# Performance work log

Measured on AMD Instinct MI355X. Metric: run time of the kernel, lower is better.

## Reference

```python
import jax, jax.numpy as jnp
import numpy as np

N, E, G = 50000, 500000, 64
DIN, ED, H1, H2, HD, OUT = 128, 32, 256, 128, 64, 8


def setup_inputs() -> dict:
    key = jax.random.key(0)
    ks = jax.random.split(key, 20)
    g = lambda i, shape: (jax.random.normal(ks[i], shape, jnp.float32) * 0.05)
    return dict(
        node_attr=jax.random.normal(ks[0], (N, DIN), jnp.float32),
        edge_attr=jax.random.normal(ks[1], (E, ED), jnp.float32),
        edge_src=jax.random.randint(ks[2], (E,), 0, N, jnp.int32),
        edge_dst=jax.random.randint(ks[3], (E,), 0, N, jnp.int32),
        batch=jnp.sort(jax.random.randint(ks[4], (N,), 0, G, jnp.int32)),
        Wl1=g(5, (DIN, H1)), bl1=jnp.zeros((H1,), jnp.float32),
        Wr1=g(6, (DIN, H1)), br1=jnp.zeros((H1,), jnp.float32),
        We1=g(7, (ED, H1)), att1=g(8, (H1,)), b1=jnp.zeros((H1,), jnp.float32),
        Wl2=g(9, (H1, H2)), bl2=jnp.zeros((H2,), jnp.float32),
        Wr2=g(10, (H1, H2)), br2=jnp.zeros((H2,), jnp.float32),
        We2=g(11, (ED, H2)), att2=g(12, (H2,)), b2=jnp.zeros((H2,), jnp.float32),
        Wd1=g(13, (H2, HD)), bd1=jnp.zeros((HD,), jnp.float32),
        bn_gamma=jnp.ones((HD,), jnp.float32), bn_beta=jnp.zeros((HD,), jnp.float32),
        bn_mean=jnp.zeros((HD,), jnp.float32), bn_var=jnp.ones((HD,), jnp.float32),
        Wd2=g(14, (HD, OUT)), bd2=jnp.zeros((OUT,), jnp.float32),
    )


def gatv2(x, src, dst, eattr, Wl, bl, Wr, br, We, att, bias, n):
    # PyG GATv2Conv, heads=1: add self-loops (fill_value='mean' for edge_attr)
    ones = jnp.ones((eattr.shape[0],), x.dtype)
    deg = jax.ops.segment_sum(ones, dst, n)
    loop_attr = jax.ops.segment_sum(eattr, dst, n) / jnp.maximum(deg, 1.0)[:, None]
    loop = jnp.arange(n, dtype=src.dtype)
    src_ = jnp.concatenate([src, loop])
    dst_ = jnp.concatenate([dst, loop])
    eattr_ = jnp.concatenate([eattr, loop_attr], axis=0)
    xl = x @ Wl + bl  # [n, C] source transform (lin_l)
    xr = x @ Wr + br  # [n, C] dest transform (lin_r)
    # edge-wise GATv2 score: a^T LeakyReLU(xl_j + xr_i + We e_ij)
    e = jax.nn.leaky_relu(xl[src_] + xr[dst_] + eattr_ @ We, 0.2) @ att  # [E+n]
    m = jax.ops.segment_max(e, dst_, n)
    w = jnp.exp(e - m[dst_])
    denom = jax.ops.segment_sum(w, dst_, n)
    alpha = w / denom[dst_]
    return jax.ops.segment_sum(alpha[:, None] * xl[src_], dst_, n) + bias


def reference(node_attr, edge_attr, edge_src, edge_dst, batch,
              Wl1, bl1, Wr1, br1, We1, att1, b1,
              Wl2, bl2, Wr2, br2, We2, att2, b2,
              Wd1, bd1, bn_gamma, bn_beta, bn_mean, bn_var, Wd2, bd2):
    x = jax.nn.relu(gatv2(node_attr, edge_src, edge_dst, edge_attr,
                          Wl1, bl1, Wr1, br1, We1, att1, b1, N))
    x = jax.nn.relu(gatv2(x, edge_src, edge_dst, edge_attr,
                          Wl2, bl2, Wr2, br2, We2, att2, b2, N))
    # global mean pool over graphs
    cnt = jax.ops.segment_sum(jnp.ones((N,), x.dtype), batch, G)
    x = jax.ops.segment_sum(x, batch, G) / jnp.maximum(cnt, 1.0)[:, None]
    x = x @ Wd1 + bd1
    # BatchNorm1d in eval mode (running stats); dropout is identity in eval
    x = (x - bn_mean) / jnp.sqrt(bn_var + 1e-5) * bn_gamma + bn_beta
    x = jax.nn.leaky_relu(x, 0.1)
    return x @ Wd2 + bd2
```

## Files before the change

kernel.cpp:

```cpp
#include <hip/hip_runtime.h>
#include <cstdint>
#include <cstddef>

constexpr int Nn = 50000;
constexpr int Ne = 500000;
constexpr int Gg = 64;
constexpr int DIN = 128, ED = 32, H1 = 256, H2 = 128, HD = 64, NOUT = 8;

__global__ void count_deg_kernel(const int* __restrict__ dst, int* __restrict__ deg) {
    int e = blockIdx.x * 256 + threadIdx.x;
    if (e < Ne) atomicAdd(&deg[dst[e]], 1);
}

__global__ __launch_bounds__(1024) void scan_kernel(const int* __restrict__ deg,
                                                    int* __restrict__ row_start) {
    __shared__ int part[1024];
    int t = threadIdx.x;
    const int chunk = (Nn + 1023) / 1024;
    int lo = t * chunk;
    int hi = min(lo + chunk, Nn);
    int s = 0;
    for (int i = lo; i < hi; i++) s += deg[i];
    part[t] = s;
    __syncthreads();
    for (int off = 1; off < 1024; off <<= 1) {
        int add = (t >= off) ? part[t - off] : 0;
        __syncthreads();
        part[t] += add;
        __syncthreads();
    }
    int base = (t == 0) ? 0 : part[t - 1];
    for (int i = lo; i < hi; i++) { row_start[i] = base; base += deg[i]; }
    if (t == 0) row_start[Nn] = Ne;
}

__global__ void scatter_kernel(const int* __restrict__ dst, const int* __restrict__ row_start,
                               int* __restrict__ cursor, int* __restrict__ perm) {
    int e = blockIdx.x * 256 + threadIdx.x;
    if (e < Ne) {
        int d = dst[e];
        int p = atomicAdd(&cursor[d], 1);
        perm[row_start[d] + p] = e;
    }
}

__global__ void build_sd_kernel(const int* __restrict__ perm, const int* __restrict__ src,
                                const int* __restrict__ dst,
                                int* __restrict__ srcv, int* __restrict__ dstv) {
    int j = blockIdx.x * 256 + threadIdx.x;
    if (j < Ne) {
        int e = perm[j];
        srcv[j] = src[e];
        dstv[j] = dst[e];
    }
}

__global__ void loop_attr_kernel(const int* __restrict__ row_start, const int* __restrict__ perm,
                                 const float* __restrict__ eattr, float* __restrict__ loop_attr) {
    int tid = blockIdx.x * 256 + threadIdx.x;
    if (tid >= Nn * 8) return;
    int i = tid >> 3, q = (tid & 7) << 2;
    int r0 = row_start[i], r1 = row_start[i + 1];
    float4 s = make_float4(0.f, 0.f, 0.f, 0.f);
    for (int j = r0; j < r1; j++) {
        int e = perm[j];
        float4 v = *(const float4*)(eattr + (size_t)e * ED + q);
        s.x += v.x; s.y += v.y; s.z += v.z; s.w += v.w;
    }
    float inv = 1.0f / fmaxf((float)(r1 - r0), 1.0f);
    *(float4*)(loop_attr + (size_t)i * ED + q) =
        make_float4(s.x * inv, s.y * inv, s.z * inv, s.w * inv);
}

__global__ __launch_bounds__(256) void gemm_bias2_kernel(const float* __restrict__ A,
                                                         const float* __restrict__ W0,
                                                         const float* __restrict__ bias0,
                                                         float* __restrict__ C0,
                                                         const float* __restrict__ W1,
                                                         const float* __restrict__ bias1,
                                                         float* __restrict__ C1,
                                                         int M, int K, int Ncols) {
    const float* W = blockIdx.z ? W1 : W0;
    const float* bias = blockIdx.z ? bias1 : bias0;
    float* C = blockIdx.z ? C1 : C0;
    __shared__ float As[16][68];
    __shared__ float Bs[16][68];
    const int m0 = blockIdx.y * 64, n0 = blockIdx.x * 64;
    const int tid = threadIdx.x;
    const int tx = tid & 15, ty = tid >> 4;
    float acc[4][4] = {};
    const int ar = tid >> 2, ac4 = (tid & 3) << 2;
    const int br = tid >> 4, bc4 = (tid & 15) << 2;
    const bool arow_ok = (m0 + ar < M);

    float4 av = make_float4(0.f, 0.f, 0.f, 0.f);
    if (arow_ok) av = *(const float4*)(A + (size_t)(m0 + ar) * K + ac4);
    float4 bv = *(const float4*)(W + (size_t)br * Ncols + n0 + bc4);

    for (int k0 = 0; k0 < K; k0 += 16) {
        As[ac4 + 0][ar] = av.x; As[ac4 + 1][ar] = av.y;
        As[ac4 + 2][ar] = av.z; As[ac4 + 3][ar] = av.w;
        *(float4*)&Bs[br][bc4] = bv;
        __syncthreads();
        if (k0 + 16 < K) {
            if (arow_ok) av = *(const float4*)(A + (size_t)(m0 + ar) * K + k0 + 16 + ac4);
            bv = *(const float4*)(W + (size_t)(k0 + 16 + br) * Ncols + n0 + bc4);
        }
#pragma unroll
        for (int k = 0; k < 16; k++) {
            float a[4], b[4];
#pragma unroll
            for (int i = 0; i < 4; i++) a[i] = As[k][ty * 4 + i];
#pragma unroll
            for (int j = 0; j < 4; j++) b[j] = Bs[k][tx * 4 + j];
#pragma unroll
            for (int i = 0; i < 4; i++)
#pragma unroll
                for (int j = 0; j < 4; j++) acc[i][j] = fmaf(a[i], b[j], acc[i][j]);
        }
        __syncthreads();
    }
#pragma unroll
    for (int i = 0; i < 4; i++) {
        int m = m0 + ty * 4 + i;
        if (m < M) {
            float4 o;
            o.x = acc[i][0] + bias[n0 + tx * 4 + 0];
            o.y = acc[i][1] + bias[n0 + tx * 4 + 1];
            o.z = acc[i][2] + bias[n0 + tx * 4 + 2];
            o.w = acc[i][3] + bias[n0 + tx * 4 + 3];
            *(float4*)(C + (size_t)m * Ncols + n0 + tx * 4) = o;
        }
    }
}

template <int C>
__global__ __launch_bounds__(256) void score_gemm2_kernel(
    int count, const int* __restrict__ perm,
    const int* __restrict__ srcv, const int* __restrict__ dstv,
    const float* __restrict__ attr,
    const float* __restrict__ xl, const float* __restrict__ xr,
    const float* __restrict__ We, const float* __restrict__ att,
    float* __restrict__ sc_out) {
    __shared__ float As[32][68];
    __shared__ float Bs[32][68];
    const int m0 = blockIdx.x * 64;
    const int tid = threadIdx.x, tx = tid & 15, ty = tid >> 4;

    {
        int ar = tid >> 2, ac8 = (tid & 3) << 3;
        int row = min(m0 + ar, count - 1);
        int e = perm ? perm[row] : row;
        const float* s = attr + (size_t)e * ED + ac8;
        float4 v0 = *(const float4*)s;
        float4 v1 = *(const float4*)(s + 4);
        As[ac8 + 0][ar] = v0.x; As[ac8 + 1][ar] = v0.y;
        As[ac8 + 2][ar] = v0.z; As[ac8 + 3][ar] = v0.w;
        As[ac8 + 4][ar] = v1.x; As[ac8 + 5][ar] = v1.y;
        As[ac8 + 6][ar] = v1.z; As[ac8 + 7][ar] = v1.w;
    }

    int rs[4], rd[4];
#pragma unroll
    for (int i = 0; i < 4; i++) {
        int j = min(m0 + ty * 4 + i, count - 1);
        rs[i] = srcv ? srcv[j] : j;
        rd[i] = dstv ? dstv[j] : j;
    }

    float p[4] = {0.f, 0.f, 0.f, 0.f};

    for (int n0 = 0; n0 < C; n0 += 64) {
        {
            int br = tid >> 3, bc8 = (tid & 7) << 3;
            const float* s = We + (size_t)br * C + n0 + bc8;
            *(float4*)&Bs[br][bc8] = *(const float4*)s;
            *(float4*)&Bs[br][bc8 + 4] = *(const float4*)(s + 4);
        }
        __syncthreads();

        float acc[4][4] = {};
#pragma unroll
        for (int k = 0; k < ED; k++) {
            float4 av = *(const float4*)&As[k][ty * 4];
            float4 bv = *(const float4*)&Bs[k][tx * 4];
            float a[4] = {av.x, av.y, av.z, av.w};
            float b[4] = {bv.x, bv.y, bv.z, bv.w};
#pragma unroll
            for (int i = 0; i < 4; i++)
#pragma unroll
                for (int j = 0; j < 4; j++) acc[i][j] = fmaf(a[i], b[j], acc[i][j]);
        }

        float attv[4];
#pragma unroll
        for (int j = 0; j < 4; j++) attv[j] = att[n0 + tx * 4 + j];
#pragma unroll
        for (int i = 0; i < 4; i++) {
            float4 a4 = *(const float4*)(xl + (size_t)rs[i] * C + n0 + tx * 4);
            float4 b4 = *(const float4*)(xr + (size_t)rd[i] * C + n0 + tx * 4);
            float xs4[4] = {a4.x + b4.x, a4.y + b4.y, a4.z + b4.z, a4.w + b4.w};
#pragma unroll
            for (int j = 0; j < 4; j++) {
                float v = acc[i][j] + xs4[j];
                v = v > 0.f ? v : 0.2f * v;
                p[i] = fmaf(v, attv[j], p[i]);
            }
        }
        __syncthreads();
    }

#pragma unroll
    for (int i = 0; i < 4; i++) {
        float q = p[i];
        q += __shfl_xor(q, 1);
        q += __shfl_xor(q, 2);
        q += __shfl_xor(q, 4);
        q += __shfl_xor(q, 8);
        int r = m0 + ty * 4 + i;
        if (tx == 0 && r < count) sc_out[r] = q;
    }
}

template <int C>
__global__ __launch_bounds__(256) void aggregate2_kernel(
    const int* __restrict__ row_start, const int* __restrict__ srcv,
    const float* __restrict__ scores, const float* __restrict__ sscore,
    const float* __restrict__ xl, const float* __restrict__ bias,
    float* __restrict__ xout) {
    constexpr int VP = C / 64;
    const int wave = threadIdx.x >> 6, lane = threadIdx.x & 63;
    const int i = blockIdx.x * 4 + wave;
    if (i >= Nn) return;
    const int r0 = row_start[i], r1 = row_start[i + 1];

    float mx = sscore[i];
    for (int j = r0 + lane; j < r1; j += 64) mx = fmaxf(mx, scores[j]);
#pragma unroll
    for (int off = 32; off >= 1; off >>= 1) mx = fmaxf(mx, __shfl_xor(mx, off));

    float l = 0.f;
    float acc[VP];
#pragma unroll
    for (int j = 0; j < VP; j++) acc[j] = 0.f;

    float wA[4], xA[4][VP];
    auto load_batch = [&](int j0, float* w, float (*x)[VP]) {
#pragma unroll
        for (int q = 0; q < 4; q++) {
            int j = min(j0 + q, r1 - 1);
            w[q] = scores[j];
            const float* p = xl + (size_t)srcv[j] * C + lane * VP;
            if constexpr (VP == 4) {
                float4 v = *(const float4*)p;
                x[q][0] = v.x; x[q][1] = v.y; x[q][2] = v.z; x[q][3] = v.w;
            } else {
                float2 v = *(const float2*)p;
                x[q][0] = v.x; x[q][1] = v.y;
            }
        }
    };
    if (r0 < r1) load_batch(r0, wA, xA);

    for (int j0 = r0; j0 < r1; j0 += 4) {
        float wB[4], xB[4][VP];
        if (j0 + 4 < r1) load_batch(j0 + 4, wB, xB);
        const int nb = min(4, r1 - j0);
        for (int q = 0; q < nb; q++) {
            float w = __expf(wA[q] - mx);
            l += w;
#pragma unroll
            for (int j = 0; j < VP; j++) acc[j] = fmaf(w, xA[q][j], acc[j]);
        }
        if (j0 + 4 < r1) {
#pragma unroll
            for (int q = 0; q < 4; q++) {
                wA[q] = wB[q];
#pragma unroll
                for (int j = 0; j < VP; j++) xA[q][j] = xB[q][j];
            }
        }
    }

    {
        float w = __expf(sscore[i] - mx);
        l += w;
        const float* p = xl + (size_t)i * C + lane * VP;
        if constexpr (VP == 4) {
            float4 v = *(const float4*)p;
            acc[0] = fmaf(w, v.x, acc[0]); acc[1] = fmaf(w, v.y, acc[1]);
            acc[2] = fmaf(w, v.z, acc[2]); acc[3] = fmaf(w, v.w, acc[3]);
        } else {
            float2 v = *(const float2*)p;
            acc[0] = fmaf(w, v.x, acc[0]); acc[1] = fmaf(w, v.y, acc[1]);
        }
    }

    float invl = 1.0f / l;
    float* xo = xout + (size_t)i * C + lane * VP;
    if constexpr (VP == 4) {
        float4 bv = *(const float4*)(bias + lane * 4);
        float4 o;
        o.x = fmaxf(fmaf(acc[0], invl, bv.x), 0.f);
        o.y = fmaxf(fmaf(acc[1], invl, bv.y), 0.f);
        o.z = fmaxf(fmaf(acc[2], invl, bv.z), 0.f);
        o.w = fmaxf(fmaf(acc[3], invl, bv.w), 0.f);
        *(float4*)xo = o;
    } else {
        float2 bv = *(const float2*)(bias + lane * 2);
        float2 o;
        o.x = fmaxf(fmaf(acc[0], invl, bv.x), 0.f);
        o.y = fmaxf(fmaf(acc[1], invl, bv.y), 0.f);
        *(float2*)xo = o;
    }
}

__global__ __launch_bounds__(128) void pool2_kernel(const float* __restrict__ x2,
                                                    const int* __restrict__ batch,
                                                    float* __restrict__ pooled,
                                                    float* __restrict__ cnt) {
    const int c = threadIdx.x;
    const int chunk = (Nn + gridDim.x - 1) / gridDim.x;
    int lo = blockIdx.x * chunk;
    int hi = min(lo + chunk, Nn);
    if (lo >= hi) return;
    int gcur = batch[lo];
    float acc = 0.f, ncnt = 0.f;
    for (int i = lo; i < hi; i++) {
        int g = batch[i];
        if (g != gcur) {
            atomicAdd(&pooled[gcur * H2 + c], acc);
            if (c == 0) atomicAdd(&cnt[gcur], ncnt);
            acc = 0.f; ncnt = 0.f; gcur = g;
        }
        acc += x2[(size_t)i * H2 + c];
        ncnt += 1.f;
    }
    atomicAdd(&pooled[gcur * H2 + c], acc);
    if (c == 0) atomicAdd(&cnt[gcur], ncnt);
}

__global__ __launch_bounds__(64) void head_kernel(
    const float* __restrict__ pooled, const float* __restrict__ cnt,
    const float* __restrict__ Wd1, const float* __restrict__ bd1,
    const float* __restrict__ gamma, const float* __restrict__ beta,
    const float* __restrict__ mean, const float* __restrict__ var,
    const float* __restrict__ Wd2, const float* __restrict__ bd2,
    float* __restrict__ out) {
    __shared__ float xm[H2];
    __shared__ float h[HD];
    int g = blockIdx.x, t = threadIdx.x;
    float c = fmaxf(cnt[g], 1.0f);
    for (int i = t; i < H2; i += 64) xm[i] = pooled[g * H2 + i] / c;
    __syncthreads();
    float a = bd1[t];
    for (int k = 0; k < H2; k++) a = fmaf(xm[k], Wd1[k * HD + t], a);
    a = (a - mean[t]) / sqrtf(var[t] + 1e-5f) * gamma[t] + beta[t];
    a = a > 0.f ? a : 0.1f * a;
    h[t] = a;
    __syncthreads();
    if (t < NOUT) {
        float o = bd2[t];
        for (int k = 0; k < HD; k++) o = fmaf(h[k], Wd2[k * NOUT + t], o);
        out[g * NOUT + t] = o;
    }
}

extern "C" void kernel_launch(void* const* d_in, const int* in_sizes, int n_in,
                              void* d_out, int out_size, void* d_ws, size_t ws_size,
                              hipStream_t stream) {
    const float* node_attr = (const float*)d_in[0];
    const float* edge_attr = (const float*)d_in[1];
    const int* edge_src = (const int*)d_in[2];
    const int* edge_dst = (const int*)d_in[3];
    const int* batch = (const int*)d_in[4];
    const float* Wl1 = (const float*)d_in[5];  const float* bl1 = (const float*)d_in[6];
    const float* Wr1 = (const float*)d_in[7];  const float* br1 = (const float*)d_in[8];
    const float* We1 = (const float*)d_in[9];  const float* att1 = (const float*)d_in[10];
    const float* b1 = (const float*)d_in[11];
    const float* Wl2 = (const float*)d_in[12]; const float* bl2 = (const float*)d_in[13];
    const float* Wr2 = (const float*)d_in[14]; const float* br2 = (const float*)d_in[15];
    const float* We2 = (const float*)d_in[16]; const float* att2 = (const float*)d_in[17];
    const float* b2 = (const float*)d_in[18];
    const float* Wd1 = (const float*)d_in[19]; const float* bd1 = (const float*)d_in[20];
    const float* bn_gamma = (const float*)d_in[21]; const float* bn_beta = (const float*)d_in[22];
    const float* bn_mean = (const float*)d_in[23];  const float* bn_var = (const float*)d_in[24];
    const float* Wd2 = (const float*)d_in[25]; const float* bd2 = (const float*)d_in[26];
    float* out = (float*)d_out;

    char* ws = (char*)d_ws;
    size_t off = 0;
    auto alloc = [&](size_t bytes) -> char* {
        char* p = ws + off;
        off = (off + bytes + 255) & ~(size_t)255;
        return p;
    };
    int* deg         = (int*)alloc((size_t)Nn * 4);
    int* row_start   = (int*)alloc((size_t)(Nn + 1) * 4);
    int* cursor      = (int*)alloc((size_t)Nn * 4);
    int* perm        = (int*)alloc((size_t)Ne * 4);
    int* srcv        = (int*)alloc((size_t)Ne * 4);
    int* dstv        = (int*)alloc((size_t)Ne * 4);
    float* loop_attr = (float*)alloc((size_t)Nn * ED * 4);
    float* scores    = (float*)alloc((size_t)Ne * 4);
    float* sscore    = (float*)alloc((size_t)Nn * 4);
    float* pooled    = (float*)alloc((size_t)Gg * H2 * 4);
    float* cnt       = (float*)alloc((size_t)Gg * 4);
    float* xlb       = (float*)alloc((size_t)Nn * H1 * 4);
    float* xrb       = (float*)alloc((size_t)Nn * H1 * 4);
    float* x1        = (float*)alloc((size_t)Nn * H1 * 4);

    hipMemsetAsync(deg, 0, (size_t)Nn * 4, stream);
    hipMemsetAsync(cursor, 0, (size_t)Nn * 4, stream);
    hipMemsetAsync(pooled, 0, (size_t)Gg * H2 * 4, stream);
    hipMemsetAsync(cnt, 0, (size_t)Gg * 4, stream);

    count_deg_kernel<<<(Ne + 255) / 256, 256, 0, stream>>>(edge_dst, deg);
    scan_kernel<<<1, 1024, 0, stream>>>(deg, row_start);
    scatter_kernel<<<(Ne + 255) / 256, 256, 0, stream>>>(edge_dst, row_start, cursor, perm);
    build_sd_kernel<<<(Ne + 255) / 256, 256, 0, stream>>>(perm, edge_src, edge_dst, srcv, dstv);
    loop_attr_kernel<<<(Nn * 8 + 255) / 256, 256, 0, stream>>>(row_start, perm, edge_attr, loop_attr);

    const int eb = (Ne + 63) / 64, nbk = (Nn + 63) / 64;

    gemm_bias2_kernel<<<dim3(H1 / 64, (Nn + 63) / 64, 2), 256, 0, stream>>>(
        node_attr, Wl1, bl1, xlb, Wr1, br1, xrb, Nn, DIN, H1);
    score_gemm2_kernel<H1><<<eb, 256, 0, stream>>>(
        Ne, perm, srcv, dstv, edge_attr, xlb, xrb, We1, att1, scores);
    score_gemm2_kernel<H1><<<nbk, 256, 0, stream>>>(
        Nn, nullptr, nullptr, nullptr, loop_attr, xlb, xrb, We1, att1, sscore);
    aggregate2_kernel<H1><<<(Nn + 3) / 4, 256, 0, stream>>>(
        row_start, srcv, scores, sscore, xlb, b1, x1);

    gemm_bias2_kernel<<<dim3(H2 / 64, (Nn + 63) / 64, 2), 256, 0, stream>>>(
        x1, Wl2, bl2, xlb, Wr2, br2, xrb, Nn, H1, H2);
    score_gemm2_kernel<H2><<<eb, 256, 0, stream>>>(
        Ne, perm, srcv, dstv, edge_attr, xlb, xrb, We2, att2, scores);
    score_gemm2_kernel<H2><<<nbk, 256, 0, stream>>>(
        Nn, nullptr, nullptr, nullptr, loop_attr, xlb, xrb, We2, att2, sscore);
    float* x2 = x1;
    aggregate2_kernel<H2><<<(Nn + 3) / 4, 256, 0, stream>>>(
        row_start, srcv, scores, sscore, xlb, b2, x2);

    pool2_kernel<<<256, 128, 0, stream>>>(x2, batch, pooled, cnt);
    head_kernel<<<Gg, 64, 0, stream>>>(pooled, cnt, Wd1, bd1, bn_gamma, bn_beta,
                                       bn_mean, bn_var, Wd2, bd2, out);
}
```

Measured before the change: 935.1 us.

## Fuse edge score computation and softmax aggregation into one online-softmax kernel

Replaces the separate edge-score GEMM kernels (edges and self-loops) and the aggregation kernel with one wave-per-node kernel. Each wave keeps We in registers, computes every in-edge's score on the fly and accumulates with an online softmax. This removes the score buffers and the re-read of xl rows between kernels. In exchange, each edge's 32-wide edge_attr row is now read with scalar-broadcast loads per wave, the wave does a 64-lane shuffle reduction for every edge, and the large register array for We (128 floats for H1) may lower occupancy.

```diff
diff --git a/kernel.cpp b/kernel.cpp
--- a/kernel.cpp
+++ b/kernel.cpp
@@ -1,6 +1,7 @@
 #include <hip/hip_runtime.h>
 #include <cstdint>
 #include <cstddef>
+#include <cmath>
 
 constexpr int Nn = 50000;
 constexpr int Ne = 500000;
@@ -135,171 +136,117 @@
 }
 
 template <int C>
-__global__ __launch_bounds__(256) void score_gemm2_kernel(
-    int count, const int* __restrict__ perm,
-    const int* __restrict__ srcv, const int* __restrict__ dstv,
-    const float* __restrict__ attr,
+__global__ __launch_bounds__(256) void fused_gat_kernel(
+    const int* __restrict__ row_start, const int* __restrict__ srcv,
+    const int* __restrict__ perm,
+    const float* __restrict__ eattr, const float* __restrict__ loop_attr,
     const float* __restrict__ xl, const float* __restrict__ xr,
     const float* __restrict__ We, const float* __restrict__ att,
-    float* __restrict__ sc_out) {
-    __shared__ float As[32][68];
-    __shared__ float Bs[32][68];
-    const int m0 = blockIdx.x * 64;
-    const int tid = threadIdx.x, tx = tid & 15, ty = tid >> 4;
-
-    {
-        int ar = tid >> 2, ac8 = (tid & 3) << 3;
-        int row = min(m0 + ar, count - 1);
-        int e = perm ? perm[row] : row;
-        const float* s = attr + (size_t)e * ED + ac8;
-        float4 v0 = *(const float4*)s;
-        float4 v1 = *(const float4*)(s + 4);
-        As[ac8 + 0][ar] = v0.x; As[ac8 + 1][ar] = v0.y;
-        As[ac8 + 2][ar] = v0.z; As[ac8 + 3][ar] = v0.w;
-        As[ac8 + 4][ar] = v1.x; As[ac8 + 5][ar] = v1.y;
-        As[ac8 + 6][ar] = v1.z; As[ac8 + 7][ar] = v1.w;
-    }
-
-    int rs[4], rd[4];
-#pragma unroll
-    for (int i = 0; i < 4; i++) {
-        int j = min(m0 + ty * 4 + i, count - 1);
-        rs[i] = srcv ? srcv[j] : j;
-        rd[i] = dstv ? dstv[j] : j;
-    }
-
-    float p[4] = {0.f, 0.f, 0.f, 0.f};
-
-    for (int n0 = 0; n0 < C; n0 += 64) {
-        {
-            int br = tid >> 3, bc8 = (tid & 7) << 3;
-            const float* s = We + (size_t)br * C + n0 + bc8;
-            *(float4*)&Bs[br][bc8] = *(const float4*)s;
-            *(float4*)&Bs[br][bc8 + 4] = *(const float4*)(s + 4);
-        }
-        __syncthreads();
-
-        float acc[4][4] = {};
-#pragma unroll
-        for (int k = 0; k < ED; k++) {
-            float4 av = *(const float4*)&As[k][ty * 4];
-            float4 bv = *(const float4*)&Bs[k][tx * 4];
-            float a[4] = {av.x, av.y, av.z, av.w};
-            float b[4] = {bv.x, bv.y, bv.z, bv.w};
-#pragma unroll
-            for (int i = 0; i < 4; i++)
-#pragma unroll
-                for (int j = 0; j < 4; j++) acc[i][j] = fmaf(a[i], b[j], acc[i][j]);
-        }
-
-        float attv[4];
-#pragma unroll
-        for (int j = 0; j < 4; j++) attv[j] = att[n0 + tx * 4 + j];
-#pragma unroll
-        for (int i = 0; i < 4; i++) {
-            float4 a4 = *(const float4*)(xl + (size_t)rs[i] * C + n0 + tx * 4);
-            float4 b4 = *(const float4*)(xr + (size_t)rd[i] * C + n0 + tx * 4);
-            float xs4[4] = {a4.x + b4.x, a4.y + b4.y, a4.z + b4.z, a4.w + b4.w};
-#pragma unroll
-            for (int j = 0; j < 4; j++) {
-                float v = acc[i][j] + xs4[j];
-                v = v > 0.f ? v : 0.2f * v;
-                p[i] = fmaf(v, attv[j], p[i]);
-            }
-        }
-        __syncthreads();
-    }
-
-#pragma unroll
-    for (int i = 0; i < 4; i++) {
-        float q = p[i];
-        q += __shfl_xor(q, 1);
-        q += __shfl_xor(q, 2);
-        q += __shfl_xor(q, 4);
-        q += __shfl_xor(q, 8);
-        int r = m0 + ty * 4 + i;
-        if (tx == 0 && r < count) sc_out[r] = q;
-    }
-}
-
-template <int C>
-__global__ __launch_bounds__(256) void aggregate2_kernel(
-    const int* __restrict__ row_start, const int* __restrict__ srcv,
-    const float* __restrict__ scores, const float* __restrict__ sscore,
-    const float* __restrict__ xl, const float* __restrict__ bias,
-    float* __restrict__ xout) {
-    constexpr int VP = C / 64;
+    const float* __restrict__ bias, float* __restrict__ xout) {
+    constexpr int CPL = C / 64;
     const int wave = threadIdx.x >> 6, lane = threadIdx.x & 63;
     const int i = blockIdx.x * 4 + wave;
     if (i >= Nn) return;
+    const int c0 = lane * CPL;
+
+    float wreg[ED][CPL];
+#pragma unroll
+    for (int k = 0; k < ED; k++) {
+        if constexpr (CPL == 4) {
+            float4 v = *(const float4*)(We + (size_t)k * C + c0);
+            wreg[k][0] = v.x; wreg[k][1] = v.y; wreg[k][2] = v.z; wreg[k][3] = v.w;
+        } else {
+            float2 v = *(const float2*)(We + (size_t)k * C + c0);
+            wreg[k][0] = v.x; wreg[k][1] = v.y;
+        }
+    }
+    float attv[CPL];
+#pragma unroll
+    for (int c = 0; c < CPL; c++) attv[c] = att[c0 + c];
+
     const int r0 = row_start[i], r1 = row_start[i + 1];
 
-    float mx = sscore[i];
-    for (int j = r0 + lane; j < r1; j += 64) mx = fmaxf(mx, scores[j]);
-#pragma unroll
-    for (int off = 32; off >= 1; off >>= 1) mx = fmaxf(mx, __shfl_xor(mx, off));
-
-    float l = 0.f;
-    float acc[VP];
-#pragma unroll
-    for (int j = 0; j < VP; j++) acc[j] = 0.f;
-
-    float wA[4], xA[4][VP];
-    auto load_batch = [&](int j0, float* w, float (*x)[VP]) {
-#pragma unroll
-        for (int q = 0; q < 4; q++) {
-            int j = min(j0 + q, r1 - 1);
-            w[q] = scores[j];
-            const float* p = xl + (size_t)srcv[j] * C + lane * VP;
-            if constexpr (VP == 4) {
-                float4 v = *(const float4*)p;
-                x[q][0] = v.x; x[q][1] = v.y; x[q][2] = v.z; x[q][3] = v.w;
-            } else {
-                float2 v = *(const float2*)p;
-                x[q][0] = v.x; x[q][1] = v.y;
-            }
-        }
-    };
-    if (r0 < r1) load_batch(r0, wA, xA);
-
-    for (int j0 = r0; j0 < r1; j0 += 4) {
-        float wB[4], xB[4][VP];
-        if (j0 + 4 < r1) load_batch(j0 + 4, wB, xB);
-        const int nb = min(4, r1 - j0);
-        for (int q = 0; q < nb; q++) {
-            float w = __expf(wA[q] - mx);
-            l += w;
-#pragma unroll
-            for (int j = 0; j < VP; j++) acc[j] = fmaf(w, xA[q][j], acc[j]);
-        }
-        if (j0 + 4 < r1) {
-#pragma unroll
-            for (int q = 0; q < 4; q++) {
-                wA[q] = wB[q];
-#pragma unroll
-                for (int j = 0; j < VP; j++) xA[q][j] = xB[q][j];
-            }
-        }
-    }
+    auto load_x = [&](const float* rowbase, float (&xs)[CPL]) {
+        if constexpr (CPL == 4) {
+            float4 v = *(const float4*)(rowbase + c0);
+            xs[0] = v.x; xs[1] = v.y; xs[2] = v.z; xs[3] = v.w;
+        } else {
+            float2 v = *(const float2*)(rowbase + c0);
+            xs[0] = v.x; xs[1] = v.y;
+        }
+    };
+    auto load_ea = [&](const float* rowbase, float4 (&ea)[8]) {
+#pragma unroll
+        for (int q = 0; q < 8; q++) ea[q] = *(const float4*)(rowbase + q * 4);
+    };
+
+    float xri[CPL];
+    load_x(xr + (size_t)i * C, xri);
+
+    float m = -INFINITY, l = 0.f;
+    float acc[CPL] = {};
+
+    auto process = [&](const float4 (&ea)[8], const float (&xls)[CPL]) {
+        float ew[CPL] = {};
+#pragma unroll
+        for (int q = 0; q < 8; q++) {
+            const float eak[4] = {ea[q].x, ea[q].y, ea[q].z, ea[q].w};
+#pragma unroll
+            for (int t = 0; t < 4; t++)
+#pragma unroll
+                for (int c = 0; c < CPL; c++)
+                    ew[c] = fmaf(eak[t], wreg[q * 4 + t][c], ew[c]);
+        }
+        float pp = 0.f;
+#pragma unroll
+        for (int c = 0; c < CPL; c++) {
+            float v = ew[c] + xls[c] + xri[c];
+            v = v > 0.f ? v : 0.2f * v;
+            pp = fmaf(v, attv[c], pp);
+        }
+        pp += __shfl_xor(pp, 1);  pp += __shfl_xor(pp, 2);
+        pp += __shfl_xor(pp, 4);  pp += __shfl_xor(pp, 8);
+        pp += __shfl_xor(pp, 16); pp += __shfl_xor(pp, 32);
+        float mn = fmaxf(m, pp);
+        float sc = __expf(m - mn);
+        float w  = __expf(pp - mn);
+        l = fmaf(l, sc, w);
+#pragma unroll
+        for (int c = 0; c < CPL; c++) acc[c] = fmaf(acc[c], sc, w * xls[c]);
+        m = mn;
+    };
 
     {
-        float w = __expf(sscore[i] - mx);
-        l += w;
-        const float* p = xl + (size_t)i * C + lane * VP;
-        if constexpr (VP == 4) {
-            float4 v = *(const float4*)p;
-            acc[0] = fmaf(w, v.x, acc[0]); acc[1] = fmaf(w, v.y, acc[1]);
-            acc[2] = fmaf(w, v.z, acc[2]); acc[3] = fmaf(w, v.w, acc[3]);
-        } else {
-            float2 v = *(const float2*)p;
-            acc[0] = fmaf(w, v.x, acc[0]); acc[1] = fmaf(w, v.y, acc[1]);
+        float xli[CPL];
+        load_x(xl + (size_t)i * C, xli);
+        float4 eaS[8];
+        load_ea(loop_attr + (size_t)i * ED, eaS);
+        process(eaS, xli);
+    }
+
+    float4 eaA[8], eaB[8];
+    float xlA[CPL], xlB[CPL];
+    auto load_edge = [&](int j, float4 (&ea)[8], float (&xs)[CPL]) {
+        int e = perm[j];
+        int s = srcv[j];
+        load_ea(eattr + (size_t)e * ED, ea);
+        load_x(xl + (size_t)s * C, xs);
+    };
+    if (r0 < r1) load_edge(r0, eaA, xlA);
+    for (int j = r0; j < r1; j += 2) {
+        const bool hasB = (j + 1 < r1);
+        if (hasB) load_edge(j + 1, eaB, xlB);
+        process(eaA, xlA);
+        if (hasB) {
+            if (j + 2 < r1) load_edge(j + 2, eaA, xlA);
+            process(eaB, xlB);
         }
     }
 
     float invl = 1.0f / l;
-    float* xo = xout + (size_t)i * C + lane * VP;
-    if constexpr (VP == 4) {
-        float4 bv = *(const float4*)(bias + lane * 4);
+    float* xo = xout + (size_t)i * C + c0;
+    if constexpr (CPL == 4) {
+        float4 bv = *(const float4*)(bias + c0);
         float4 o;
         o.x = fmaxf(fmaf(acc[0], invl, bv.x), 0.f);
         o.y = fmaxf(fmaf(acc[1], invl, bv.y), 0.f);
@@ -307,7 +254,7 @@
         o.w = fmaxf(fmaf(acc[3], invl, bv.w), 0.f);
         *(float4*)xo = o;
     } else {
-        float2 bv = *(const float2*)(bias + lane * 2);
+        float2 bv = *(const float2*)(bias + c0);
         float2 o;
         o.x = fmaxf(fmaf(acc[0], invl, bv.x), 0.f);
         o.y = fmaxf(fmaf(acc[1], invl, bv.y), 0.f);
@@ -402,8 +349,6 @@
     int* srcv        = (int*)alloc((size_t)Ne * 4);
     int* dstv        = (int*)alloc((size_t)Ne * 4);
     float* loop_attr = (float*)alloc((size_t)Nn * ED * 4);
-    float* scores    = (float*)alloc((size_t)Ne * 4);
-    float* sscore    = (float*)alloc((size_t)Nn * 4);
     float* pooled    = (float*)alloc((size_t)Gg * H2 * 4);
     float* cnt       = (float*)alloc((size_t)Gg * 4);
     float* xlb       = (float*)alloc((size_t)Nn * H1 * 4);
@@ -421,26 +366,18 @@
     build_sd_kernel<<<(Ne + 255) / 256, 256, 0, stream>>>(perm, edge_src, edge_dst, srcv, dstv);
     loop_attr_kernel<<<(Nn * 8 + 255) / 256, 256, 0, stream>>>(row_start, perm, edge_attr, loop_attr);
 
-    const int eb = (Ne + 63) / 64, nbk = (Nn + 63) / 64;
+    const int fb = (Nn + 3) / 4;
 
     gemm_bias2_kernel<<<dim3(H1 / 64, (Nn + 63) / 64, 2), 256, 0, stream>>>(
         node_attr, Wl1, bl1, xlb, Wr1, br1, xrb, Nn, DIN, H1);
-    score_gemm2_kernel<H1><<<eb, 256, 0, stream>>>(
-        Ne, perm, srcv, dstv, edge_attr, xlb, xrb, We1, att1, scores);
-    score_gemm2_kernel<H1><<<nbk, 256, 0, stream>>>(
-        Nn, nullptr, nullptr, nullptr, loop_attr, xlb, xrb, We1, att1, sscore);
-    aggregate2_kernel<H1><<<(Nn + 3) / 4, 256, 0, stream>>>(
-        row_start, srcv, scores, sscore, xlb, b1, x1);
+    fused_gat_kernel<H1><<<fb, 256, 0, stream>>>(
+        row_start, srcv, perm, edge_attr, loop_attr, xlb, xrb, We1, att1, b1, x1);
 
     gemm_bias2_kernel<<<dim3(H2 / 64, (Nn + 63) / 64, 2), 256, 0, stream>>>(
         x1, Wl2, bl2, xlb, Wr2, br2, xrb, Nn, H1, H2);
-    score_gemm2_kernel<H2><<<eb, 256, 0, stream>>>(
-        Ne, perm, srcv, dstv, edge_attr, xlb, xrb, We2, att2, scores);
-    score_gemm2_kernel<H2><<<nbk, 256, 0, stream>>>(
-        Nn, nullptr, nullptr, nullptr, loop_attr, xlb, xrb, We2, att2, sscore);
     float* x2 = x1;
-    aggregate2_kernel<H2><<<(Nn + 3) / 4, 256, 0, stream>>>(
-        row_start, srcv, scores, sscore, xlb, b2, x2);
+    fused_gat_kernel<H2><<<fb, 256, 0, stream>>>(
+        row_start, srcv, perm, edge_attr, loop_attr, xlb, xrb, We2, att2, b2, x2);
 
     pool2_kernel<<<256, 128, 0, stream>>>(x2, batch, pooled, cnt);
     head_kernel<<<Gg, 64, 0, stream>>>(pooled, cnt, Wd1, bd1, bn_gamma, bn_beta,
```

After: 1.262 ms. 35.0% more time.

## Compute edge-attribute score GEMM with split-bf16 MFMA instead of FP32 FMA

Applied to the files above, without the earlier changes.

Replaces the FP32 shared-memory edge score GEMM with a kernel that uses bf16 MFMA 16x16x32. It keeps near-FP32 accuracy by splitting each operand into high and low bf16 parts and issuing three MFMAs per tile. The xl/xr gather is loaded straight into the accumulators, and the per-wave partial dot products with att are combined through shared memory. This adds conversion kernels that pre-split edge_attr, loop_attr and the transposed We, which costs extra memory traffic on 500k×32 attributes each call. The per-lane gathers of xl/xr are now scalar rather than float4, which may hurt memory efficiency.

```diff
diff --git a/kernel.cpp b/kernel.cpp
--- a/kernel.cpp
+++ b/kernel.cpp
@@ -1,11 +1,24 @@
 #include <hip/hip_runtime.h>
 #include <cstdint>
 #include <cstddef>
+#include <cmath>
 
 constexpr int Nn = 50000;
 constexpr int Ne = 500000;
 constexpr int Gg = 64;
 constexpr int DIN = 128, ED = 32, H1 = 256, H2 = 128, HD = 64, NOUT = 8;
+
+typedef __attribute__((ext_vector_type(8))) short bf16x8;
+typedef __attribute__((ext_vector_type(4))) float f32x4;
+
+__device__ __forceinline__ unsigned short f2bf(float x) {
+    unsigned u = __float_as_uint(x);
+    u += 0x7FFFu + ((u >> 16) & 1u);
+    return (unsigned short)(u >> 16);
+}
+__device__ __forceinline__ float bf2f(unsigned short h) {
+    return __uint_as_float(((unsigned)h) << 16);
+}
 
 __global__ void count_deg_kernel(const int* __restrict__ dst, int* __restrict__ deg) {
     int e = blockIdx.x * 256 + threadIdx.x;
@@ -70,6 +83,35 @@
     float inv = 1.0f / fmaxf((float)(r1 - r0), 1.0f);
     *(float4*)(loop_attr + (size_t)i * ED + q) =
         make_float4(s.x * inv, s.y * inv, s.z * inv, s.w * inv);
+}
+
+__global__ void cvt_split_kernel(const float* __restrict__ src,
+                                 unsigned short* __restrict__ hi,
+                                 unsigned short* __restrict__ lo, int n4) {
+    int idx = blockIdx.x * 256 + threadIdx.x;
+    if (idx >= n4) return;
+    float4 v = *(const float4*)(src + (size_t)idx * 4);
+    float x[4] = {v.x, v.y, v.z, v.w};
+    unsigned short h[4], l[4];
+#pragma unroll
+    for (int c = 0; c < 4; c++) {
+        h[c] = f2bf(x[c]);
+        l[c] = f2bf(x[c] - bf2f(h[c]));
+    }
+    *(ushort4*)(hi + (size_t)idx * 4) = make_ushort4(h[0], h[1], h[2], h[3]);
+    *(ushort4*)(lo + (size_t)idx * 4) = make_ushort4(l[0], l[1], l[2], l[3]);
+}
+
+__global__ void cvt_W_kernel(const float* __restrict__ We,
+                             unsigned short* __restrict__ whi,
+                             unsigned short* __restrict__ wlo, int C) {
+    int t = blockIdx.x * 256 + threadIdx.x;
+    if (t >= C * ED) return;
+    int c = t >> 5, k = t & 31;
+    float x = We[(size_t)k * C + c];
+    unsigned short h = f2bf(x);
+    whi[t] = h;
+    wlo[t] = f2bf(x - bf2f(h));
 }
 
 __global__ __launch_bounds__(256) void gemm_bias2_kernel(const float* __restrict__ A,
@@ -135,90 +177,110 @@
 }
 
 template <int C>
-__global__ __launch_bounds__(256) void score_gemm2_kernel(
+__global__ void score_mfma_kernel(
     int count, const int* __restrict__ perm,
     const int* __restrict__ srcv, const int* __restrict__ dstv,
-    const float* __restrict__ attr,
+    const unsigned short* __restrict__ ehi, const unsigned short* __restrict__ elo,
     const float* __restrict__ xl, const float* __restrict__ xr,
-    const float* __restrict__ We, const float* __restrict__ att,
-    float* __restrict__ sc_out) {
-    __shared__ float As[32][68];
-    __shared__ float Bs[32][68];
-    const int m0 = blockIdx.x * 64;
-    const int tid = threadIdx.x, tx = tid & 15, ty = tid >> 4;
-
-    {
-        int ar = tid >> 2, ac8 = (tid & 3) << 3;
-        int row = min(m0 + ar, count - 1);
-        int e = perm ? perm[row] : row;
-        const float* s = attr + (size_t)e * ED + ac8;
-        float4 v0 = *(const float4*)s;
-        float4 v1 = *(const float4*)(s + 4);
-        As[ac8 + 0][ar] = v0.x; As[ac8 + 1][ar] = v0.y;
-        As[ac8 + 2][ar] = v0.z; As[ac8 + 3][ar] = v0.w;
-        As[ac8 + 4][ar] = v1.x; As[ac8 + 5][ar] = v1.y;
-        As[ac8 + 6][ar] = v1.z; As[ac8 + 7][ar] = v1.w;
-    }
-
-    int rs[4], rd[4];
-#pragma unroll
-    for (int i = 0; i < 4; i++) {
-        int j = min(m0 + ty * 4 + i, count - 1);
-        rs[i] = srcv ? srcv[j] : j;
-        rd[i] = dstv ? dstv[j] : j;
-    }
-
-    float p[4] = {0.f, 0.f, 0.f, 0.f};
-
-    for (int n0 = 0; n0 < C; n0 += 64) {
-        {
-            int br = tid >> 3, bc8 = (tid & 7) << 3;
-            const float* s = We + (size_t)br * C + n0 + bc8;
-            *(float4*)&Bs[br][bc8] = *(const float4*)s;
-            *(float4*)&Bs[br][bc8 + 4] = *(const float4*)(s + 4);
-        }
-        __syncthreads();
-
-        float acc[4][4] = {};
-#pragma unroll
-        for (int k = 0; k < ED; k++) {
-            float4 av = *(const float4*)&As[k][ty * 4];
-            float4 bv = *(const float4*)&Bs[k][tx * 4];
-            float a[4] = {av.x, av.y, av.z, av.w};
-            float b[4] = {bv.x, bv.y, bv.z, bv.w};
-#pragma unroll
-            for (int i = 0; i < 4; i++)
-#pragma unroll
-                for (int j = 0; j < 4; j++) acc[i][j] = fmaf(a[i], b[j], acc[i][j]);
-        }
-
-        float attv[4];
-#pragma unroll
-        for (int j = 0; j < 4; j++) attv[j] = att[n0 + tx * 4 + j];
-#pragma unroll
-        for (int i = 0; i < 4; i++) {
-            float4 a4 = *(const float4*)(xl + (size_t)rs[i] * C + n0 + tx * 4);
-            float4 b4 = *(const float4*)(xr + (size_t)rd[i] * C + n0 + tx * 4);
-            float xs4[4] = {a4.x + b4.x, a4.y + b4.y, a4.z + b4.z, a4.w + b4.w};
-#pragma unroll
-            for (int j = 0; j < 4; j++) {
-                float v = acc[i][j] + xs4[j];
-                v = v > 0.f ? v : 0.2f * v;
-                p[i] = fmaf(v, attv[j], p[i]);
+    const unsigned short* __restrict__ wthi, const unsigned short* __restrict__ wtlo,
+    const float* __restrict__ att, float* __restrict__ sc_out) {
+    constexpr int WPB = C / 64;
+    constexpr int NTHR = WPB * 64;
+    __shared__ unsigned short Ah[64 * 40], Al[64 * 40];
+    __shared__ unsigned short Bh[C * 40], Bl[C * 40];
+    __shared__ float pw[WPB][64];
+    const int tid = threadIdx.x;
+    const int j0 = blockIdx.x * 64;
+
+    for (int t = tid; t < 64 * 4; t += NTHR) {
+        int row = t >> 2, part = t & 3;
+        int j = min(j0 + row, count - 1);
+        int e = perm ? perm[j] : j;
+        *(uint4*)&Ah[row * 40 + part * 8] = *(const uint4*)(ehi + (size_t)e * ED + part * 8);
+        *(uint4*)&Al[row * 40 + part * 8] = *(const uint4*)(elo + (size_t)e * ED + part * 8);
+    }
+    for (int t = tid; t < C * 4; t += NTHR) {
+        int col = t >> 2, part = t & 3;
+        *(uint4*)&Bh[col * 40 + part * 8] = *(const uint4*)(wthi + (size_t)col * ED + part * 8);
+        *(uint4*)&Bl[col * 40 + part * 8] = *(const uint4*)(wtlo + (size_t)col * ED + part * 8);
+    }
+    __syncthreads();
+
+    const int wv = tid >> 6, lane = tid & 63;
+    const int g = lane >> 4, li = lane & 15;
+    const int colbase = wv * 64 + li;
+
+    float attv[4];
+#pragma unroll
+    for (int n = 0; n < 4; n++) attv[n] = att[colbase + n * 16];
+
+    int sE[4][4], dE[4][4];
+#pragma unroll
+    for (int m = 0; m < 4; m++)
+#pragma unroll
+        for (int r = 0; r < 4; r++) {
+            int j = min(j0 + m * 16 + g * 4 + r, count - 1);
+            sE[m][r] = srcv ? srcv[j] : j;
+            dE[m][r] = dstv ? dstv[j] : j;
+        }
+
+    f32x4 acc[4][4];
+#pragma unroll
+    for (int m = 0; m < 4; m++)
+#pragma unroll
+        for (int n = 0; n < 4; n++) {
+            int col = colbase + n * 16;
+#pragma unroll
+            for (int r = 0; r < 4; r++)
+                acc[m][n][r] = xl[(size_t)sE[m][r] * C + col] + xr[(size_t)dE[m][r] * C + col];
+        }
+
+    bf16x8 af_h[4], af_l[4], bf_h[4], bf_l[4];
+#pragma unroll
+    for (int m = 0; m < 4; m++) {
+        af_h[m] = *(const bf16x8*)&Ah[(m * 16 + li) * 40 + g * 8];
+        af_l[m] = *(const bf16x8*)&Al[(m * 16 + li) * 40 + g * 8];
+    }
+#pragma unroll
+    for (int n = 0; n < 4; n++) {
+        int col = colbase + n * 16;
+        bf_h[n] = *(const bf16x8*)&Bh[col * 40 + g * 8];
+        bf_l[n] = *(const bf16x8*)&Bl[col * 40 + g * 8];
+    }
+
+#pragma unroll
+    for (int m = 0; m < 4; m++)
+#pragma unroll
+        for (int n = 0; n < 4; n++) {
+            acc[m][n] = __builtin_amdgcn_mfma_f32_16x16x32_bf16(af_h[m], bf_h[n], acc[m][n], 0, 0, 0);
+            acc[m][n] = __builtin_amdgcn_mfma_f32_16x16x32_bf16(af_h[m], bf_l[n], acc[m][n], 0, 0, 0);
+            acc[m][n] = __builtin_amdgcn_mfma_f32_16x16x32_bf16(af_l[m], bf_h[n], acc[m][n], 0, 0, 0);
+        }
+
+#pragma unroll
+    for (int m = 0; m < 4; m++)
+#pragma unroll
+        for (int r = 0; r < 4; r++) {
+            float s = 0.f;
+#pragma unroll
+            for (int n = 0; n < 4; n++) {
+                float z = acc[m][n][r];
+                z = z > 0.f ? z : 0.2f * z;
+                s = fmaf(z, attv[n], s);
             }
-        }
-        __syncthreads();
-    }
-
-#pragma unroll
-    for (int i = 0; i < 4; i++) {
-        float q = p[i];
-        q += __shfl_xor(q, 1);
-        q += __shfl_xor(q, 2);
-        q += __shfl_xor(q, 4);
-        q += __shfl_xor(q, 8);
-        int r = m0 + ty * 4 + i;
-        if (tx == 0 && r < count) sc_out[r] = q;
+            s += __shfl_xor(s, 1);
+            s += __shfl_xor(s, 2);
+            s += __shfl_xor(s, 4);
+            s += __shfl_xor(s, 8);
+            if (li == 0) pw[wv][m * 16 + g * 4 + r] = s;
+        }
+    __syncthreads();
+    if (tid < 64) {
+        float s = pw[0][tid];
+#pragma unroll
+        for (int w = 1; w < WPB; w++) s += pw[w][tid];
+        int j = j0 + tid;
+        if (j < count) sc_out[j] = s;
     }
 }
 
@@ -409,6 +471,14 @@
     float* xlb       = (float*)alloc((size_t)Nn * H1 * 4);
     float* xrb       = (float*)alloc((size_t)Nn * H1 * 4);
     float* x1        = (float*)alloc((size_t)Nn * H1 * 4);
+    unsigned short* ehi = (unsigned short*)alloc((size_t)Ne * ED * 2);
+    unsigned short* elo = (unsigned short*)alloc((size_t)Ne * ED * 2);
+    unsigned short* lhi = (unsigned short*)alloc((size_t)Nn * ED * 2);
+    unsigned short* llo = (unsigned short*)alloc((size_t)Nn * ED * 2);
+    unsigned short* w1hi = (unsigned short*)alloc((size_t)H1 * ED * 2);
+    unsigned short* w1lo = (unsigned short*)alloc((size_t)H1 * ED * 2);
+    unsigned short* w2hi = (unsigned short*)alloc((size_t)H2 * ED * 2);
+    unsigned short* w2lo = (unsigned short*)alloc((size_t)H2 * ED * 2);
 
     hipMemsetAsync(deg, 0, (size_t)Nn * 4, stream);
     hipMemsetAsync(cursor, 0, (size_t)Nn * 4, stream);
@@ -421,23 +491,28 @@
     build_sd_kernel<<<(Ne + 255) / 256, 256, 0, stream>>>(perm, edge_src, edge_dst, srcv, dstv);
     loop_attr_kernel<<<(Nn * 8 + 255) / 256, 256, 0, stream>>>(row_start, perm, edge_attr, loop_attr);
 
-    const int eb = (Ne + 63) / 64, nbk = (Nn + 63) / 64;
+    cvt_split_kernel<<<(Ne * 8 + 255) / 256, 256, 0, stream>>>(edge_attr, ehi, elo, Ne * 8);
+    cvt_split_kernel<<<(Nn * 8 + 255) / 256, 256, 0, stream>>>(loop_attr, lhi, llo, Nn * 8);
+    cvt_W_kernel<<<(H1 * ED + 255) / 256, 256, 0, stream>>>(We1, w1hi, w1lo, H1);
+    cvt_W_kernel<<<(H2 * ED + 255) / 256, 256, 0, stream>>>(We2, w2hi, w2lo, H2);
+
+    const int eb64 = (Ne + 63) / 64, nb64 = (Nn + 63) / 64;
 
     gemm_bias2_kernel<<<dim3(H1 / 64, (Nn + 63) / 64, 2), 256, 0, stream>>>(
         node_attr, Wl1, bl1, xlb, Wr1, br1, xrb, Nn, DIN, H1);
-    score_gemm2_kernel<H1><<<eb, 256, 0, stream>>>(
-        Ne, perm, srcv, dstv, edge_attr, xlb, xrb, We1, att1, scores);
-    score_gemm2_kernel<H1><<<nbk, 256, 0, stream>>>(
-        Nn, nullptr, nullptr, nullptr, loop_attr, xlb, xrb, We1, att1, sscore);
+    score_mfma_kernel<H1><<<eb64, 256, 0, stream>>>(
+        Ne, perm, srcv, dstv, ehi, elo, xlb, xrb, w1hi, w1lo, att1, scores);
+    score_mfma_kernel<H1><<<nb64, 256, 0, stream>>>(
+        Nn, nullptr, nullptr, nullptr, lhi, llo, xlb, xrb, w1hi, w1lo, att1, sscore);
     aggregate2_kernel<H1><<<(Nn + 3) / 4, 256, 0, stream>>>(
         row_start, srcv, scores, sscore, xlb, b1, x1);
 
     gemm_bias2_kernel<<<dim3(H2 / 64, (Nn + 63) / 64, 2), 256, 0, stream>>>(
         x1, Wl2, bl2, xlb, Wr2, br2, xrb, Nn, H1, H2);
-    score_gemm2_kernel<H2><<<eb, 256, 0, stream>>>(
-        Ne, perm, srcv, dstv, edge_attr, xlb, xrb, We2, att2, scores);
-    score_gemm2_kernel<H2><<<nbk, 256, 0, stream>>>(
-        Nn, nullptr, nullptr, nullptr, loop_attr, xlb, xrb, We2, att2, sscore);
+    score_mfma_kernel<H2><<<eb64, 128, 0, stream>>>(
+        Ne, perm, srcv, dstv, ehi, elo, xlb, xrb, w2hi, w2lo, att2, scores);
+    score_mfma_kernel<H2><<<nb64, 128, 0, stream>>>(
+        Nn, nullptr, nullptr, nullptr, lhi, llo, xlb, xrb, w2hi, w2lo, att2, sscore);
     float* x2 = x1;
     aggregate2_kernel<H2><<<(Nn + 3) / 4, 256, 0, stream>>>(
         row_start, srcv, scores, sscore, xlb, b2, x2);
```

New measurement: 1.079 ms. 15.4% more time.
